# Optimization experiments

Hardware: AMD Instinct MI355X
Metric: run time of the kernel (lower is better)

## Reference

```python
import jax, jax.numpy as jnp
import numpy as np

GROUPS = 16
EPS = 1e-6


def group_norm(x, gamma, beta):
    b, c, h, w = x.shape
    xg = x.reshape(b, GROUPS, c // GROUPS, h, w)
    mean = xg.mean(axis=(2, 3, 4), keepdims=True)
    var = xg.var(axis=(2, 3, 4), keepdims=True)
    xn = ((xg - mean) * jax.lax.rsqrt(var + EPS)).reshape(b, c, h, w)
    return xn * gamma[None, :, None, None] + beta[None, :, None, None]


def conv1x1(x, w, b):
    # x: [B,C,H,W], w: [O,C], b: [O]
    return jnp.einsum('bchw,oc->bohw', x, w) + b[None, :, None, None]


def setup_inputs() -> dict:
    key = jax.random.key(0)
    ks = jax.random.split(key, 10)
    C = 256
    x = jax.random.normal(ks[0], (4, C, 64, 64), dtype=jnp.float32)
    s = 1.0 / np.sqrt(C)
    return {
        'x': x,
        'gamma': jnp.ones((C,), jnp.float32),
        'beta': jnp.zeros((C,), jnp.float32),
        'wq': jax.random.normal(ks[1], (C, C), jnp.float32) * s,
        'bq': jnp.zeros((C,), jnp.float32),
        'wk': jax.random.normal(ks[2], (C, C), jnp.float32) * s,
        'bk': jnp.zeros((C,), jnp.float32),
        'wv': jax.random.normal(ks[3], (C, C), jnp.float32) * s,
        'bv': jnp.zeros((C,), jnp.float32),
        'wp': jax.random.normal(ks[4], (C, C), jnp.float32) * s,
        'bp': jnp.zeros((C,), jnp.float32),
    }


def reference(x, gamma, beta, wq, bq, wk, bk, wv, bv, wp, bp):
    b, c, h, w = x.shape
    hn = group_norm(x, gamma, beta)
    q = conv1x1(hn, wq, bq).reshape(b, c, h * w)   # [B,C,N]
    k = conv1x1(hn, wk, bk).reshape(b, c, h * w)
    v = conv1x1(hn, wv, bv).reshape(b, c, h * w)
    # scores[b,i,j] = sum_c q[b,c,i] * k[b,c,j], scaled by c^-0.5
    scores = jnp.einsum('bci,bcj->bij', q, k) * (c ** -0.5)
    attn = jax.nn.softmax(scores, axis=2)           # [B,N,N]
    # h_out[b,c,i] = sum_j v[b,c,j] * attn[b,i,j]
    h_out = jnp.einsum('bcj,bij->bci', v, attn).reshape(b, c, h, w)
    return x + conv1x1(h_out, wp, bp)
```

## Files before the change

### kernel.cpp

```cpp
#include <hip/hip_runtime.h>

#define B_ 4
#define C_ 256
#define N_ 4096
#define K2_ 0.09016844f
#define THR_ 64.0f

typedef __attribute__((ext_vector_type(8))) short short8;
typedef __attribute__((ext_vector_type(4))) float f32x4;
typedef __attribute__((ext_vector_type(16))) float f32x16;
typedef __attribute__((ext_vector_type(4))) unsigned int uint4v;

static __device__ __forceinline__ short f2bf(float f) {
  union { float f; unsigned u; } v; v.f = f;
  unsigned r = v.u + 0x7FFFu + ((v.u >> 16) & 1u);
  return (short)(r >> 16);
}
static __device__ __forceinline__ float bf2f(short s) {
  union { unsigned u; float f; } v; v.u = ((unsigned)(unsigned short)s) << 16;
  return v.f;
}
static __device__ __forceinline__ f32x4 mfma16(short8 a, short8 b, f32x4 c) {
  return __builtin_amdgcn_mfma_f32_16x16x32_bf16(a, b, c, 0, 0, 0);
}
static __device__ __forceinline__ f32x16 mfma32(short8 a, short8 b, f32x16 c) {
  return __builtin_amdgcn_mfma_f32_32x32x16_bf16(a, b, c, 0, 0, 0);
}
static __device__ __forceinline__ unsigned cvtpk(float lo, float hi) {
  unsigned r;
  asm("v_cvt_pk_bf16_f32 %0, %1, %2" : "=v"(r) : "v"(lo), "v"(hi));
  return r;
}
static __device__ __forceinline__ void plswap(unsigned& a, unsigned& b) {
  asm volatile("v_permlane32_swap_b32 %0, %1" : "+v"(a), "+v"(b));
}
static __device__ __forceinline__ void gload16(const void* g, void* l) {
  __builtin_amdgcn_global_load_lds(
      (const __attribute__((address_space(1))) unsigned int*)g,
      (__attribute__((address_space(3))) unsigned int*)l, 16, 0, 0);
}

__global__ __launch_bounds__(256) void gn_stats1(const float* __restrict__ x,
                                                 float2* __restrict__ part) {
  int bg = blockIdx.x >> 2, ch = blockIdx.x & 3;
  const float* xp = x + (long)bg * 65536 + ch * 16384;
  int t = threadIdx.x, lane = t & 63, w = t >> 6;
  float s = 0.f, ss = 0.f;
  for (int e = t * 4; e < 16384; e += 1024) {
    f32x4 v = *(const f32x4*)(xp + e);
    s += (v[0] + v[1]) + (v[2] + v[3]);
    ss += (v[0] * v[0] + v[1] * v[1]) + (v[2] * v[2] + v[3] * v[3]);
  }
  for (int off = 1; off < 64; off <<= 1) {
    s += __shfl_xor(s, off);
    ss += __shfl_xor(ss, off);
  }
  __shared__ float rs[4], rq[4];
  if (lane == 0) { rs[w] = s; rq[w] = ss; }
  __syncthreads();
  if (t == 0)
    part[blockIdx.x] = make_float2((rs[0] + rs[1]) + (rs[2] + rs[3]),
                                   (rq[0] + rq[1]) + (rq[2] + rq[3]));
}

__global__ __launch_bounds__(256) void gn_norm(const float* __restrict__ x,
                                               const float* __restrict__ gamma,
                                               const float* __restrict__ beta,
                                               const float2* __restrict__ part,
                                               short* __restrict__ hn) {
  int ic = blockIdx.x, g = blockIdx.y, b = blockIdx.z;
  int bg = b * 16 + g;
  float2 q0 = part[bg * 4], q1 = part[bg * 4 + 1], q2 = part[bg * 4 + 2], q3 = part[bg * 4 + 3];
  float s = (q0.x + q1.x) + (q2.x + q3.x);
  float ss = (q0.y + q1.y) + (q2.y + q3.y);
  float mean = s * (1.f / 65536.f);
  float rstd = rsqrtf(ss * (1.f / 65536.f) - mean * mean + 1e-6f);
  int t = threadIdx.x;
  int i = ic * 256 + t;
  __shared__ short Ls[16][256];
#pragma unroll
  for (int cl = 0; cl < 16; cl++) {
    int c = g * 16 + cl;
    float v = x[((long)(b * 256 + c)) * N_ + i];
    Ls[cl][t] = f2bf((v - mean) * rstd * gamma[c] + beta[c]);
  }
  __syncthreads();
  short8 v0, v1;
#pragma unroll
  for (int q = 0; q < 8; q++) { v0[q] = Ls[q][t]; v1[q] = Ls[8 + q][t]; }
  short* dst = hn + ((long)b * N_ + ic * 256 + t) * C_ + g * 16;
  *(short8*)dst = v0;
  *(short8*)(dst + 8) = v1;
}

__global__ __launch_bounds__(256) void cast_w(const float* __restrict__ wq,
                                              const float* __restrict__ wk,
                                              const float* __restrict__ wv,
                                              const float* __restrict__ wp,
                                              short* __restrict__ out) {
  int idx = blockIdx.x * 256 + threadIdx.x;
  int which = idx >> 16, e = idx & 65535;
  const float* src = which == 0 ? wq : which == 1 ? wk : which == 2 ? wv : wp;
  out[(which << 16) + e] = f2bf(src[e]);
}

__global__ __launch_bounds__(256) void gemm_qkv(const short* __restrict__ hn,
                                                const short* __restrict__ wqkv,
                                                const float* __restrict__ bq,
                                                const float* __restrict__ bk,
                                                const float* __restrict__ bv,
                                                short* __restrict__ qT,
                                                short* __restrict__ kT,
                                                short* __restrict__ vbM) {
  __shared__ __align__(16) short As[2][128 * 32];
  __shared__ __align__(16) short Bs[2][128 * 32];
  const int bz = blockIdx.z;
  const int n0 = blockIdx.x * 128;
  const int m0 = blockIdx.y * 128;
  const int t = threadIdx.x, lane = t & 63, w = t >> 6;
  const int wm = (w >> 1) * 64, wn = (w & 1) * 64;
  const short* Ab = hn + (long)bz * N_ * C_;
  f32x4 acc[4][4];
#pragma unroll
  for (int m = 0; m < 4; m++)
#pragma unroll
    for (int n = 0; n < 4; n++) acc[m][n] = (f32x4)0.f;
  const int g16 = (lane >> 4) * 16;

  auto stage = [&](int kt8, int buf) {
    int kt = kt8 * 32;
#pragma unroll
    for (int s = 0; s < 2; s++) {
      int q = w * 2 + s;
      int flat = q * 1024 + lane * 16;
      int row = flat >> 6, c = flat & 63;
      int cs = c ^ ((row & 3) << 4);
      gload16((const char*)Ab + ((long)(m0 + row) * 256 + kt) * 2 + cs, (char*)As[buf] + flat);
      gload16((const char*)wqkv + ((long)(n0 + row) * 256 + kt) * 2 + cs, (char*)Bs[buf] + flat);
    }
  };

  stage(0, 0);
  __syncthreads();
  for (int kt8 = 0; kt8 < 8; kt8++) {
    int cur = kt8 & 1;
    if (kt8 < 7) stage(kt8 + 1, cur ^ 1);
    short8 af[4], bf[4];
#pragma unroll
    for (int m = 0; m < 4; m++) {
      int row = wm + m * 16 + (lane & 15);
      af[m] = *(const short8*)(&As[cur][0] + row * 32 + ((g16 ^ ((row & 3) << 4)) >> 1));
    }
#pragma unroll
    for (int n = 0; n < 4; n++) {
      int row = wn + n * 16 + (lane & 15);
      bf[n] = *(const short8*)(&Bs[cur][0] + row * 32 + ((g16 ^ ((row & 3) << 4)) >> 1));
    }
    __builtin_amdgcn_s_setprio(1);
#pragma unroll
    for (int m = 0; m < 4; m++)
#pragma unroll
      for (int n = 0; n < 4; n++) acc[m][n] = mfma16(af[m], bf[n], acc[m][n]);
    __builtin_amdgcn_s_setprio(0);
    __syncthreads();
  }

  int seg = n0 >> 8;
  const float* bias = seg == 0 ? bq : seg == 1 ? bk : bv;
#pragma unroll
  for (int m = 0; m < 4; m++)
#pragma unroll
    for (int n = 0; n < 4; n++)
#pragma unroll
      for (int r = 0; r < 4; r++) {
        int row = m0 + wm + m * 16 + ((lane >> 4) << 2) + r;
        int colg = n0 + wn + n * 16 + (lane & 15);
        int coll = colg & 255;
        float vv = acc[m][n][r] + bias[coll];
        if (seg == 2) vbM[(long)bz * N_ * C_ + (long)coll * N_ + row] = f2bf(vv);
        else (seg == 0 ? qT : kT)[(long)bz * N_ * C_ + (long)row * 256 + coll] = f2bf(vv);
      }
}

__global__ __launch_bounds__(256) void gemm_proj(const short* __restrict__ wp,
                                                 const short* __restrict__ hT,
                                                 const float* __restrict__ bp,
                                                 const float* __restrict__ x,
                                                 float* __restrict__ out) {
  __shared__ __align__(16) short As[2][128 * 32];
  __shared__ __align__(16) short Bs[2][128 * 32];
  const int bz = blockIdx.z;
  const int n0 = blockIdx.x * 128;
  const int m0 = blockIdx.y * 128;
  const int t = threadIdx.x, lane = t & 63, w = t >> 6;
  const int wm = (w >> 1) * 64, wn = (w & 1) * 64;
  const short* Bb = hT + (long)bz * N_ * C_;
  f32x4 acc[4][4];
#pragma unroll
  for (int m = 0; m < 4; m++)
#pragma unroll
    for (int n = 0; n < 4; n++) acc[m][n] = (f32x4)0.f;
  const int g16 = (lane >> 4) * 16;

  auto stage = [&](int kt8, int buf) {
    int kt = kt8 * 32;
#pragma unroll
    for (int s = 0; s < 2; s++) {
      int q = w * 2 + s;
      int flat = q * 1024 + lane * 16;
      int row = flat >> 6, c = flat & 63;
      int cs = c ^ ((row & 3) << 4);
      gload16((const char*)wp + ((long)(m0 + row) * 256 + kt) * 2 + cs, (char*)As[buf] + flat);
      gload16((const char*)Bb + ((long)(n0 + row) * 256 + kt) * 2 + cs, (char*)Bs[buf] + flat);
    }
  };

  stage(0, 0);
  __syncthreads();
  for (int kt8 = 0; kt8 < 8; kt8++) {
    int cur = kt8 & 1;
    if (kt8 < 7) stage(kt8 + 1, cur ^ 1);
    short8 af[4], bf[4];
#pragma unroll
    for (int m = 0; m < 4; m++) {
      int row = wm + m * 16 + (lane & 15);
      af[m] = *(const short8*)(&As[cur][0] + row * 32 + ((g16 ^ ((row & 3) << 4)) >> 1));
    }
#pragma unroll
    for (int n = 0; n < 4; n++) {
      int row = wn + n * 16 + (lane & 15);
      bf[n] = *(const short8*)(&Bs[cur][0] + row * 32 + ((g16 ^ ((row & 3) << 4)) >> 1));
    }
    __builtin_amdgcn_s_setprio(1);
#pragma unroll
    for (int m = 0; m < 4; m++)
#pragma unroll
      for (int n = 0; n < 4; n++) acc[m][n] = mfma16(af[m], bf[n], acc[m][n]);
    __builtin_amdgcn_s_setprio(0);
    __syncthreads();
  }

#pragma unroll
  for (int m = 0; m < 4; m++)
#pragma unroll
    for (int n = 0; n < 4; n++)
#pragma unroll
      for (int r = 0; r < 4; r++) {
        int row = m0 + wm + m * 16 + ((lane >> 4) << 2) + r;
        int col = n0 + wn + n * 16 + (lane & 15);
        long idx = (long)bz * N_ * C_ + (long)row * N_ + col;
        out[idx] = acc[m][n][r] + bp[row] + x[idx];
      }
}

__global__ __launch_bounds__(512, 2) void attn_kernel(
    const short* __restrict__ qT, const short* __restrict__ kT,
    const short* __restrict__ vM, short* __restrict__ P0, short* __restrict__ P1,
    short* __restrict__ P2, short* __restrict__ P3, float2* __restrict__ ml, int S) {
  __shared__ __align__(16) char kv[2][65536];
  __shared__ float cbr[8][32];

  const int nwg = 64 * S;
  const int id = blockIdx.x;
  const int nid = (id & 7) * (nwg >> 3) + (id >> 3);
  const int itile = nid & 15;
  const int bjs = nid >> 4;
  const int js = bjs % S;
  const int b = bjs / S;

  const int t = threadIdx.x, lane = t & 63, w = t >> 6;
  const int hi = lane >> 5, li = lane & 31;
  const int hi16 = hi * 16;
  const long bNC = (long)b * N_ * C_;
  const short* qb = qT + bNC;
  const char* kb = (const char*)(kT + bNC);
  const char* vb = (const char*)(vM + bNC);
  const int i0 = itile * 256 + w * 32;
  const int jbase = js * (N_ / S);
  const int NIT = (N_ / S) / 64;

  short8 qf[16];
  {
    const short* qp = qb + (long)(i0 + li) * C_ + hi * 8;
#pragma unroll
    for (int s = 0; s < 16; s++) qf[s] = *(const short8*)(qp + s * 16);
  }

  f32x16 acco[8];
#pragma unroll
  for (int cb = 0; cb < 8; cb++) acco[cb] = (f32x16)0.f;
  float m_run = -3e38f, l_run = 0.f;

  auto stage = [&](int it, int buf) {
    const int j0 = jbase + it * 64;
    char* Kd = kv[buf];
    char* Vd = kv[buf] + 32768;
#pragma unroll
    for (int p = 0; p < 4; p++) {
      int flat = p * 8192 + t * 16;
      int rk = flat >> 9, ck = flat & 511;
      gload16(kb + (long)(j0 + rk) * 512 + (ck ^ ((rk & 7) << 4)), Kd + flat);
      int rv = flat >> 7, cv = flat & 127;
      gload16(vb + (long)rv * (N_ * 2) + (long)j0 * 2 + (cv ^ ((rv & 7) << 4)), Vd + flat);
    }
  };

  stage(0, 0);
  __syncthreads();

  for (int it = 0; it < NIT; it++) {
    const int cur = it & 1;
    if (it + 1 < NIT) stage(it + 1, cur ^ 1);
    const char* Kb = kv[cur];
    const char* Vb = kv[cur] + 32768;

#pragma unroll
    for (int jb = 0; jb < 2; jb++) {
      f32x16 accs = (f32x16)0.f;
      const int krow = jb * 32 + li;
      const char* Kr = Kb + krow * 512;
      const int ksw = (krow & 7) << 4;
      __builtin_amdgcn_s_setprio(1);
#pragma unroll
      for (int s = 0; s < 16; s++) {
        short8 kf = *(const short8*)(Kr + ((s * 32 + hi16) ^ ksw));
        accs = mfma32(kf, qf[s], accs);
      }
      __builtin_amdgcn_s_setprio(0);

      float pmax = accs[0];
#pragma unroll
      for (int r = 1; r < 16; r++) pmax = fmaxf(pmax, accs[r]);
      pmax = fmaxf(pmax, __shfl_xor(pmax, 32));
      if (__any(pmax > m_run + THR_)) {
        float mnew = fmaxf(m_run, pmax);
        float corr = exp2f((m_run - mnew) * K2_);
        m_run = mnew;
        l_run *= corr;
        if (lane < 32) cbr[w][li] = corr;
        asm volatile("s_waitcnt lgkmcnt(0)" ::: "memory");
        f32x4 c4[4];
#pragma unroll
        for (int g = 0; g < 4; g++) c4[g] = *(const f32x4*)&cbr[w][g * 8 + hi * 4];
#pragma unroll
        for (int cb = 0; cb < 8; cb++)
#pragma unroll
          for (int r = 0; r < 16; r++) acco[cb][r] *= c4[r >> 2][r & 3];
      }
      const float mk = m_run * K2_;
      float p[16];
#pragma unroll
      for (int r = 0; r < 16; r++) {
        p[r] = exp2f(fmaf(accs[r], K2_, -mk));
        l_run += p[r];
      }

      unsigned a0 = cvtpk(p[0], p[1]), b0 = cvtpk(p[4], p[5]);
      unsigned a1 = cvtpk(p[2], p[3]), b1 = cvtpk(p[6], p[7]);
      plswap(a0, b0); plswap(a1, b1);
      uint4v u0 = {a0, a1, b0, b1};
      short8 pa0 = __builtin_bit_cast(short8, u0);
      unsigned a2 = cvtpk(p[8], p[9]), b2 = cvtpk(p[12], p[13]);
      unsigned a3 = cvtpk(p[10], p[11]), b3 = cvtpk(p[14], p[15]);
      plswap(a2, b2); plswap(a3, b3);
      uint4v u1 = {a2, a3, b2, b3};
      short8 pa1 = __builtin_bit_cast(short8, u1);

      const int jcb0 = jb * 64 + hi16;
      __builtin_amdgcn_s_setprio(1);
#pragma unroll
      for (int cb = 0; cb < 8; cb++) {
        const int vrow = cb * 32 + li;
        const char* Vr = Vb + vrow * 128;
        const int vsw = (vrow & 7) << 4;
        short8 vf0 = *(const short8*)(Vr + (jcb0 ^ vsw));
        acco[cb] = mfma32(pa0, vf0, acco[cb]);
        short8 vf1 = *(const short8*)(Vr + ((jcb0 + 32) ^ vsw));
        acco[cb] = mfma32(pa1, vf1, acco[cb]);
      }
      __builtin_amdgcn_s_setprio(0);
    }
    __syncthreads();
  }

  l_run += __shfl_xor(l_run, 32);
  float inv = 1.f / l_run;
  if (lane < 32) cbr[w][li] = inv;
  asm volatile("s_waitcnt lgkmcnt(0)" ::: "memory");
  f32x4 i4[4];
#pragma unroll
  for (int g = 0; g < 4; g++) i4[g] = *(const f32x4*)&cbr[w][g * 8 + hi * 4];

  short* Op = (js == 0) ? P0 : (js == 1) ? P1 : (js == 2) ? P2 : P3;
  short* ob = Op + bNC;
#pragma unroll
  for (int cb = 0; cb < 8; cb++)
#pragma unroll
    for (int r = 0; r < 16; r++) {
      int i = i0 + (r & 3) + 8 * (r >> 2) + 4 * hi;
      ob[(long)i * C_ + cb * 32 + li] = f2bf(acco[cb][r] * i4[r >> 2][r & 3]);
    }
  if (lane < 32)
    ml[(long)js * (B_ * N_) + b * N_ + i0 + li] = make_float2(m_run * K2_, l_run);
}

__global__ __launch_bounds__(256) void combine(const short* __restrict__ p0,
                                               const short* __restrict__ p1,
                                               const short* __restrict__ p2,
                                               const short* __restrict__ p3,
                                               const float2* __restrict__ ml, int S,
                                               short* __restrict__ hT) {
  int idx = blockIdx.x * 256 + threadIdx.x;
  int row = idx >> 5, c0 = (idx & 31) * 8;
  float2 m0 = ml[row], m1 = ml[16384 + row];
  float mmax = fmaxf(m0.x, m1.x);
  float2 m2 = m0, m3 = m0;
  if (S == 4) {
    m2 = ml[2 * 16384 + row];
    m3 = ml[3 * 16384 + row];
    mmax = fmaxf(mmax, fmaxf(m2.x, m3.x));
  }
  float w0 = m0.y * exp2f(m0.x - mmax);
  float w1 = m1.y * exp2f(m1.x - mmax);
  float w2 = 0.f, w3 = 0.f;
  if (S == 4) { w2 = m2.y * exp2f(m2.x - mmax); w3 = m3.y * exp2f(m3.x - mmax); }
  float inv = 1.f / ((w0 + w1) + (w2 + w3));
  w0 *= inv; w1 *= inv; w2 *= inv; w3 *= inv;
  long off = (long)row * 256 + c0;
  short8 u0 = *(const short8*)(p0 + off);
  short8 u1 = *(const short8*)(p1 + off);
  short8 o;
  if (S == 4) {
    short8 u2 = *(const short8*)(p2 + off);
    short8 u3 = *(const short8*)(p3 + off);
#pragma unroll
    for (int j = 0; j < 8; j++)
      o[j] = f2bf((w0 * bf2f(u0[j]) + w1 * bf2f(u1[j])) +
                  (w2 * bf2f(u2[j]) + w3 * bf2f(u3[j])));
  } else {
#pragma unroll
    for (int j = 0; j < 8; j++) o[j] = f2bf(w0 * bf2f(u0[j]) + w1 * bf2f(u1[j]));
  }
  *(short8*)(hT + off) = o;
}

extern "C" void kernel_launch(void* const* d_in, const int* in_sizes, int n_in,
                              void* d_out, int out_size, void* d_ws, size_t ws_size,
                              hipStream_t stream) {
  const float* x = (const float*)d_in[0];
  const float* gamma = (const float*)d_in[1];
  const float* beta = (const float*)d_in[2];
  const float* wq = (const float*)d_in[3];
  const float* bq = (const float*)d_in[4];
  const float* wk = (const float*)d_in[5];
  const float* bk = (const float*)d_in[6];
  const float* wv = (const float*)d_in[7];
  const float* bv = (const float*)d_in[8];
  const float* wp = (const float*)d_in[9];
  const float* bp = (const float*)d_in[10];

  char* ws = (char*)d_ws;
  short* hn = (short*)ws;
  short* qT = (short*)(ws + (size_t)8388608);
  short* kT = (short*)(ws + (size_t)16777216);
  short* vb = (short*)(ws + (size_t)25165824);
  short* wqkv = (short*)(ws + (size_t)33554432);
  short* wpb = wqkv + 3 * 65536;
  float2* part = (float2*)(ws + (size_t)34078720);
  float2* ml = (float2*)(ws + (size_t)34080768);
  short* P1 = (short*)d_out;
  short* P2 = (short*)d_out + 4194304;
  short* P3 = (short*)(ws + (size_t)34605056);
  const int S = (ws_size >= (size_t)43000000) ? 4 : 2;
  if (S == 2) { P2 = hn; P3 = hn; }

  gn_stats1<<<256, 256, 0, stream>>>(x, part);
  gn_norm<<<dim3(16, 16, 4), 256, 0, stream>>>(x, gamma, beta, part, hn);
  cast_w<<<1024, 256, 0, stream>>>(wq, wk, wv, wp, wqkv);

  gemm_qkv<<<dim3(6, 32, 4), 256, 0, stream>>>(hn, wqkv, bq, bk, bv, qT, kT, vb);

  attn_kernel<<<dim3(64 * S), 512, 0, stream>>>(qT, kT, vb, hn , P1, P2, P3, ml, S);
  combine<<<2048, 256, 0, stream>>>(hn, P1, P2, P3, ml, S, hn );

  gemm_proj<<<dim3(32, 2, 4), 256, 0, stream>>>(wpb, hn, bp, x, (float*)d_out);
}
```

Baseline: 184.1 us.

## Interleave QK of next sub-tile with PV of previous and relayout K/V LDS

Reorganizes the per-iteration 64-key tile into two 32-key halves. The QK^T MFMAs for the second half are interleaved with the PV MFMAs of the first half, so independent matrix work overlaps the softmax dependency chain. The LDS layout is changed to four 16KB regions (K0,V0,K1,V1), each with 512-byte rows and a 32-way XOR swizzle keyed on the lane row. The V tile is stored transposed-by-chunk to match. This aims to cut bank conflicts and MFMA pipeline bubbles. The cost is more complex staging address arithmetic and higher register pressure from two live score accumulators.

```diff
diff --git a/kernel.cpp b/kernel.cpp
--- a/kernel.cpp
+++ b/kernel.cpp
@@ -271,6 +271,7 @@
   const int t = threadIdx.x, lane = t & 63, w = t >> 6;
   const int hi = lane >> 5, li = lane & 31;
   const int hi16 = hi * 16;
+  const int lsw = li << 4;
   const long bNC = (long)b * N_ * C_;
   const short* qb = qT + bNC;
   const char* kb = (const char*)(kT + bNC);
@@ -293,16 +294,64 @@
 
   auto stage = [&](int it, int buf) {
     const int j0 = jbase + it * 64;
-    char* Kd = kv[buf];
-    char* Vd = kv[buf] + 32768;
-#pragma unroll
-    for (int p = 0; p < 4; p++) {
-      int flat = p * 8192 + t * 16;
-      int rk = flat >> 9, ck = flat & 511;
-      gload16(kb + (long)(j0 + rk) * 512 + (ck ^ ((rk & 7) << 4)), Kd + flat);
-      int rv = flat >> 7, cv = flat & 127;
-      gload16(vb + (long)rv * (N_ * 2) + (long)j0 * 2 + (cv ^ ((rv & 7) << 4)), Vd + flat);
-    }
+    char* Bd = kv[buf];
+#pragma unroll
+    for (int r = 0; r < 8; r++) {
+      const int region = r >> 1;
+      const int wf = (r & 1) * 8192 + t * 16;
+      char* dst = Bd + region * 16384 + wf;
+      const int jo = j0 + (region >> 1) * 32;
+      if ((region & 1) == 0) {
+        int rk = wf >> 9;
+        int cO = (wf & 511) ^ ((rk & 31) << 4);
+        gload16(kb + (long)(jo + rk) * 512 + cO, dst);
+      } else {
+        int rv = wf >> 9;
+        int cO = (wf & 511) ^ ((rv & 31) << 4);
+        int c = rv + ((cO >> 6) << 5);
+        int off = cO & 63;
+        gload16(vb + (long)c * (N_ * 2) + (long)jo * 2 + off, dst);
+      }
+    }
+  };
+
+  auto softmax_pack = [&](f32x16& accs, short8& paA, short8& paB) {
+    float pmax = accs[0];
+#pragma unroll
+    for (int r = 1; r < 16; r++) pmax = fmaxf(pmax, accs[r]);
+    pmax = fmaxf(pmax, __shfl_xor(pmax, 32));
+    if (__any(pmax > m_run + THR_)) {
+      float mnew = fmaxf(m_run, pmax);
+      float corr = exp2f((m_run - mnew) * K2_);
+      m_run = mnew;
+      l_run *= corr;
+      if (lane < 32) cbr[w][li] = corr;
+      asm volatile("s_waitcnt lgkmcnt(0)" ::: "memory");
+      f32x4 c4[4];
+#pragma unroll
+      for (int g = 0; g < 4; g++) c4[g] = *(const f32x4*)&cbr[w][g * 8 + hi * 4];
+#pragma unroll
+      for (int cb = 0; cb < 8; cb++)
+#pragma unroll
+        for (int r = 0; r < 16; r++) acco[cb][r] *= c4[r >> 2][r & 3];
+    }
+    const float mk = m_run * K2_;
+    float p[16];
+#pragma unroll
+    for (int r = 0; r < 16; r++) {
+      p[r] = exp2f(fmaf(accs[r], K2_, -mk));
+      l_run += p[r];
+    }
+    unsigned a0 = cvtpk(p[0], p[1]), b0 = cvtpk(p[4], p[5]);
+    unsigned a1 = cvtpk(p[2], p[3]), b1 = cvtpk(p[6], p[7]);
+    plswap(a0, b0); plswap(a1, b1);
+    uint4v u0 = {a0, a1, b0, b1};
+    paA = __builtin_bit_cast(short8, u0);
+    unsigned a2 = cvtpk(p[8], p[9]), b2 = cvtpk(p[12], p[13]);
+    unsigned a3 = cvtpk(p[10], p[11]), b3 = cvtpk(p[14], p[15]);
+    plswap(a2, b2); plswap(a3, b3);
+    uint4v u1 = {a2, a3, b2, b3};
+    paB = __builtin_bit_cast(short8, u1);
   };
 
   stage(0, 0);
@@ -311,75 +360,49 @@
   for (int it = 0; it < NIT; it++) {
     const int cur = it & 1;
     if (it + 1 < NIT) stage(it + 1, cur ^ 1);
-    const char* Kb = kv[cur];
-    const char* Vb = kv[cur] + 32768;
-
-#pragma unroll
-    for (int jb = 0; jb < 2; jb++) {
-      f32x16 accs = (f32x16)0.f;
-      const int krow = jb * 32 + li;
-      const char* Kr = Kb + krow * 512;
-      const int ksw = (krow & 7) << 4;
-      __builtin_amdgcn_s_setprio(1);
-#pragma unroll
-      for (int s = 0; s < 16; s++) {
-        short8 kf = *(const short8*)(Kr + ((s * 32 + hi16) ^ ksw));
-        accs = mfma32(kf, qf[s], accs);
-      }
-      __builtin_amdgcn_s_setprio(0);
-
-      float pmax = accs[0];
-#pragma unroll
-      for (int r = 1; r < 16; r++) pmax = fmaxf(pmax, accs[r]);
-      pmax = fmaxf(pmax, __shfl_xor(pmax, 32));
-      if (__any(pmax > m_run + THR_)) {
-        float mnew = fmaxf(m_run, pmax);
-        float corr = exp2f((m_run - mnew) * K2_);
-        m_run = mnew;
-        l_run *= corr;
-        if (lane < 32) cbr[w][li] = corr;
-        asm volatile("s_waitcnt lgkmcnt(0)" ::: "memory");
-        f32x4 c4[4];
-#pragma unroll
-        for (int g = 0; g < 4; g++) c4[g] = *(const f32x4*)&cbr[w][g * 8 + hi * 4];
-#pragma unroll
-        for (int cb = 0; cb < 8; cb++)
-#pragma unroll
-          for (int r = 0; r < 16; r++) acco[cb][r] *= c4[r >> 2][r & 3];
-      }
-      const float mk = m_run * K2_;
-      float p[16];
-#pragma unroll
-      for (int r = 0; r < 16; r++) {
-        p[r] = exp2f(fmaf(accs[r], K2_, -mk));
-        l_run += p[r];
-      }
-
-      unsigned a0 = cvtpk(p[0], p[1]), b0 = cvtpk(p[4], p[5]);
-      unsigned a1 = cvtpk(p[2], p[3]), b1 = cvtpk(p[6], p[7]);
-      plswap(a0, b0); plswap(a1, b1);
-      uint4v u0 = {a0, a1, b0, b1};
-      short8 pa0 = __builtin_bit_cast(short8, u0);
-      unsigned a2 = cvtpk(p[8], p[9]), b2 = cvtpk(p[12], p[13]);
-      unsigned a3 = cvtpk(p[10], p[11]), b3 = cvtpk(p[14], p[15]);
-      plswap(a2, b2); plswap(a3, b3);
-      uint4v u1 = {a2, a3, b2, b3};
-      short8 pa1 = __builtin_bit_cast(short8, u1);
-
-      const int jcb0 = jb * 64 + hi16;
-      __builtin_amdgcn_s_setprio(1);
-#pragma unroll
-      for (int cb = 0; cb < 8; cb++) {
-        const int vrow = cb * 32 + li;
-        const char* Vr = Vb + vrow * 128;
-        const int vsw = (vrow & 7) << 4;
-        short8 vf0 = *(const short8*)(Vr + (jcb0 ^ vsw));
-        acco[cb] = mfma32(pa0, vf0, acco[cb]);
-        short8 vf1 = *(const short8*)(Vr + ((jcb0 + 32) ^ vsw));
-        acco[cb] = mfma32(pa1, vf1, acco[cb]);
-      }
-      __builtin_amdgcn_s_setprio(0);
-    }
+    const char* base = kv[cur];
+    const char* Kr0 = base + li * 512;
+    const char* Vr0 = base + 16384 + li * 512;
+    const char* Kr1 = base + 32768 + li * 512;
+    const char* Vr1 = base + 49152 + li * 512;
+
+    f32x16 accs0 = (f32x16)0.f;
+    __builtin_amdgcn_s_setprio(1);
+#pragma unroll
+    for (int s = 0; s < 16; s++) {
+      short8 kf = *(const short8*)(Kr0 + ((s * 32 + hi16) ^ lsw));
+      accs0 = mfma32(kf, qf[s], accs0);
+    }
+    __builtin_amdgcn_s_setprio(0);
+    short8 pa00, pa01;
+    softmax_pack(accs0, pa00, pa01);
+
+    f32x16 accs1 = (f32x16)0.f;
+    __builtin_amdgcn_s_setprio(1);
+#pragma unroll
+    for (int u = 0; u < 8; u++) {
+      short8 kfa = *(const short8*)(Kr1 + (((2 * u) * 32 + hi16) ^ lsw));
+      accs1 = mfma32(kfa, qf[2 * u], accs1);
+      short8 vf0 = *(const short8*)(Vr0 + ((u * 64 + hi16) ^ lsw));
+      acco[u] = mfma32(pa00, vf0, acco[u]);
+      short8 kfb = *(const short8*)(Kr1 + (((2 * u + 1) * 32 + hi16) ^ lsw));
+      accs1 = mfma32(kfb, qf[2 * u + 1], accs1);
+      short8 vf1 = *(const short8*)(Vr0 + ((u * 64 + 32 + hi16) ^ lsw));
+      acco[u] = mfma32(pa01, vf1, acco[u]);
+    }
+    __builtin_amdgcn_s_setprio(0);
+    short8 pa10, pa11;
+    softmax_pack(accs1, pa10, pa11);
+
+    __builtin_amdgcn_s_setprio(1);
+#pragma unroll
+    for (int cb = 0; cb < 8; cb++) {
+      short8 vf0 = *(const short8*)(Vr1 + ((cb * 64 + hi16) ^ lsw));
+      acco[cb] = mfma32(pa10, vf0, acco[cb]);
+      short8 vf1 = *(const short8*)(Vr1 + ((cb * 64 + 32 + hi16) ^ lsw));
+      acco[cb] = mfma32(pa11, vf1, acco[cb]);
+    }
+    __builtin_amdgcn_s_setprio(0);
     __syncthreads();
   }
 
```

Measured after the change: 177.2 us. 1.04x faster.
